# Performance work log

Hardware: AMD Instinct MI355X
Metric: run time of the kernel (lower is better)

## Reference

```python
import math
import jax, jax.numpy as jnp
import numpy as np

B, N, H, NH, DD, L = 4, 384, 256, 8, 32, 4
HD = H // NH
V = 11           # num_species + 1 (padding row 0)
CUTOFF = 5.0

def _ln(x, g, b):
    m = jnp.mean(x, axis=-1, keepdims=True)
    v = jnp.mean(jnp.square(x - m), axis=-1, keepdims=True)
    return (x - m) / jnp.sqrt(v + 1e-5) * g + b

def setup_inputs() -> dict:
    key = jax.random.key(0)
    ks = iter(jax.random.split(key, 64))
    def nrm(shape, s=0.05):
        return jax.random.normal(next(ks), shape, jnp.float32) * s
    return {
        'node_indices': jax.random.randint(next(ks), (B, N), 0, V),
        'positions': jax.random.normal(next(ks), (B, N, 3), jnp.float32),
        'mask': jnp.ones((B, N), jnp.float32),
        'emb': nrm((V, H)).at[0].set(0.0),
        'ln1_g': jnp.ones((L, H)), 'ln1_b': jnp.zeros((L, H)),
        'qkv_w': nrm((L, H, 3 * H)), 'qkv_b': jnp.zeros((L, 3 * H)),
        'out_w': nrm((L, H, H)), 'out_b': jnp.zeros((L, H)),
        'rb_w1': nrm((L, DD, H)), 'rb_b1': jnp.zeros((L, H)),
        'rb_w2': nrm((L, H, NH)), 'rb_b2': jnp.zeros((L, NH)),
        'gate_w1': nrm((L, H, H)), 'gate_b1': jnp.zeros((L, H)),
        'gate_w2': nrm((L, H, H)), 'gate_b2': jnp.zeros((L, H)),
        'ln2_g': jnp.ones((L, H)), 'ln2_b': jnp.zeros((L, H)),
        'ff_w1': nrm((L, H, 2 * H)), 'ff_b1': jnp.zeros((L, 2 * H)),
        'ff_w2': nrm((L, 2 * H, H)), 'ff_b2': jnp.zeros((L, H)),
        'pool_g': jnp.ones((H,)), 'pool_beta': jnp.zeros((H,)),
        'pool_w': nrm((H, H)), 'pool_b': jnp.zeros((H,)),
        'eh_w': nrm((H, 1)), 'eh_b': jnp.zeros((1,)),
    }

def _forward(node_indices, positions, mask, emb, ln1_g, ln1_b, qkv_w, qkv_b,
             out_w, out_b, rb_w1, rb_b1, rb_w2, rb_b2, gate_w1, gate_b1,
             gate_w2, gate_b2, ln2_g, ln2_b, ff_w1, ff_b1, ff_w2, ff_b2,
             pool_g, pool_beta, pool_w, pool_b, eh_w, eh_b):
    mask_b = mask > 0
    x = emb[node_indices] * mask_b[..., None]               # [B,N,H]
    pos = positions * mask_b[..., None].astype(positions.dtype)
    rel = pos[:, :, None, :] - pos[:, None, :, :]           # [B,N,N,3]
    dist = jnp.linalg.norm(rel + 1e-9, axis=-1)             # [B,N,N]
    adj = (dist <= CUTOFF).astype(jnp.float32)
    adj = adj * mask_b[:, None, :] * mask_b[:, :, None]
    edge = adj > 0
    isolated = mask_b & ~edge.any(axis=-1)
    adj = adj + isolated.astype(jnp.float32)[:, :, None] * jnp.eye(N, dtype=jnp.float32)
    edge = adj > 0
    # Bessel envelope features [B,N,N,DD]
    kk = jnp.arange(1, DD + 1, dtype=jnp.float32)
    ang = math.pi * kk * (dist / CUTOFF)[..., None]
    feat = jnp.sin(ang) / (dist[..., None] + 1e-6)
    feat = feat * (dist <= CUTOFF)[..., None].astype(jnp.float32)
    feat = feat * adj[..., None]

    scale = math.sqrt(HD)
    NEG = jnp.finfo(jnp.float32).min
    for l in range(L):
        res = x
        h = _ln(x, ln1_g[l], ln1_b[l])
        qkv = h @ qkv_w[l] + qkv_b[l]
        q, k, v = jnp.split(qkv, 3, axis=-1)
        q = q.reshape(B, N, NH, HD)
        k = k.reshape(B, N, NH, HD)
        v = v.reshape(B, N, NH, HD)
        logits = jnp.einsum('bihd,bjhd->bhij', q, k) / scale
        hb = jax.nn.silu(feat @ rb_w1[l] + rb_b1[l])        # [B,N,N,H]
        bias = hb @ rb_w2[l] + rb_b2[l]                     # [B,N,N,NH]
        logits = logits + bias.transpose(0, 3, 1, 2)
        logits = jnp.where(edge[:, None, :, :], logits, NEG)
        attn = jax.nn.softmax(logits, axis=-1)
        ctx = jnp.einsum('bhij,bjhd->bihd', attn, v).reshape(B, N, H)
        gated = jax.nn.silu(h @ gate_w1[l] + gate_b1[l]) @ gate_w2[l] + gate_b2[l]
        x = res + ((ctx * jax.nn.sigmoid(gated)) @ out_w[l] + out_b[l])
        y = _ln(x, ln2_g[l], ln2_b[l])
        x = x + (jax.nn.gelu(y @ ff_w1[l] + ff_b1[l], approximate=False) @ ff_w2[l] + ff_b2[l])

    pooled = jax.nn.silu(_ln(x, pool_g, pool_beta) @ pool_w + pool_b)
    masked = pooled * mask_b[..., None]
    counts = jnp.maximum(jnp.sum(mask_b, axis=1), 1)
    graph = jnp.sum(masked, axis=1) / counts[:, None]
    energy = (graph @ eh_w + eh_b)[:, 0]                    # [B]
    return energy

def reference(node_indices, positions, mask, emb, ln1_g, ln1_b, qkv_w, qkv_b,
              out_w, out_b, rb_w1, rb_b1, rb_w2, rb_b2, gate_w1, gate_b1,
              gate_w2, gate_b2, ln2_g, ln2_b, ff_w1, ff_b1, ff_w2, ff_b2,
              pool_g, pool_beta, pool_w, pool_b, eh_w, eh_b):
    return _forward(node_indices, positions, mask, emb, ln1_g, ln1_b, qkv_w,
                    qkv_b, out_w, out_b, rb_w1, rb_b1, rb_w2, rb_b2, gate_w1,
                    gate_b1, gate_w2, gate_b2, ln2_g, ln2_b, ff_w1, ff_b1,
                    ff_w2, ff_b2, pool_g, pool_beta, pool_w, pool_b, eh_w, eh_b)
```

## Files before the change

kernel.cpp:

```cpp
#include <hip/hip_runtime.h>
#include <hip/hip_bf16.h>
#include <math.h>

constexpr int B_ = 4, N_ = 384, H_ = 256, NH_ = 8, DD_ = 32, L_ = 4;
constexpr int M_ = B_ * N_;
constexpr float CUT = 5.0f;
constexpr float PI_ = 3.14159265358979323846f;
constexpr float INVSC = 0.17677669529663687f;
constexpr int TBL_N = 4096;
constexpr int TBL_STRIDE = 4098;

typedef __attribute__((ext_vector_type(8))) short short8;
typedef __attribute__((ext_vector_type(4))) float f32x4;
typedef __attribute__((ext_vector_type(4))) unsigned short u16x4;
using u16 = unsigned short;

__device__ __forceinline__ u16 f2b(float f) {
  __hip_bfloat16 h = __float2bfloat16(f);
  return *reinterpret_cast<u16*>(&h);
}
__device__ __forceinline__ float b2f(u16 u) {
  __hip_bfloat16 h;
  *reinterpret_cast<u16*>(&h) = u;
  return __bfloat162float(h);
}

__device__ __forceinline__ float wave_sum(float v) {
#pragma unroll
  for (int s = 1; s < 64; s <<= 1) v += __shfl_xor(v, s);
  return v;
}


__device__ __forceinline__ void bias_item(const float* __restrict__ pos,
                                          const float* __restrict__ mask,
                                          const float* __restrict__ tbl2,
                                          u16* __restrict__ biasb, int e) {
  int j = e % N_;
  int t = e / N_;
  int i = t % N_;
  int b = t / N_;
  float mi = mask[b * N_ + i], mj = mask[b * N_ + j];
  const float* pi = pos + (size_t)(b * N_ + i) * 3;
  const float* pj = pos + (size_t)(b * N_ + j) * 3;
  float dx = pi[0] - pj[0] + 1e-9f;
  float dy = pi[1] - pj[1] + 1e-9f;
  float dz = pi[2] - pj[2] + 1e-9f;
  float d = sqrtf(dx * dx + dy * dy + dz * dz);
  bool edge = (mi > 0.f && mj > 0.f) && (d <= CUT);
  size_t plane = (size_t)N_ * N_;
  size_t obase = (size_t)b * NH_ * plane + (size_t)i * N_ + j;
  size_t lstride = (size_t)B_ * NH_ * plane;
  if (edge) {
    int ixrow;
    float fr;
    if (i == j) {
      ixrow = TBL_N + 1;
      fr = 0.f;
    } else {
      float u = d * ((float)TBL_N / CUT);
      int ix = (int)u;
      ix = ix > TBL_N - 1 ? TBL_N - 1 : ix;
      fr = u - (float)ix;
      ixrow = ix;
    }
    const float4* r0 = (const float4*)(tbl2 + (size_t)ixrow * 32);
    const float4* r1 = (const float4*)(tbl2 + (size_t)(ixrow + 1) * 32);
    float4 a0[8], a1[8];
#pragma unroll
    for (int q = 0; q < 8; q++) {
      a0[q] = r0[q];
      a1[q] = r1[q];
    }
    float w0 = 1.f - fr;
#pragma unroll
    for (int q = 0; q < 8; q++) {
      float v0[4] = {a0[q].x, a0[q].y, a0[q].z, a0[q].w};
      float v1[4] = {a1[q].x, a1[q].y, a1[q].z, a1[q].w};
#pragma unroll
      for (int c = 0; c < 4; c++) {
        int lh = q * 4 + c;
        int l = lh >> 3, h = lh & 7;
        float v = v0[c] * w0 + v1[c] * fr;
        biasb[(size_t)l * lstride + obase + (size_t)h * plane] = f2b(v);
      }
    }
  } else {
#pragma unroll
    for (int lh = 0; lh < 32; lh++) {
      int l = lh >> 3, h = lh & 7;
      biasb[(size_t)l * lstride + obase + (size_t)h * plane] = 0xFF80;
    }
  }
}

struct TrJob {
  const float* src;
  u16* dst;
  int K, N, nx, ny, nz, base, dstride;
};
struct TrJobs {
  TrJob j[7];
};
__global__ __launch_bounds__(256) void setup_all_k(TrJobs jobs,
                                                   const float* __restrict__ rb_w1,
                                                   const float* __restrict__ rb_b1,
                                                   const float* __restrict__ rb_w2,
                                                   const float* __restrict__ rb_b2,
                                                   float* __restrict__ tbl2,
                                                   const int* __restrict__ nidx,
                                                   const float* __restrict__ mask,
                                                   const float* __restrict__ emb,
                                                   float* __restrict__ X,
                                                   const float* __restrict__ l1g,
                                                   const float* __restrict__ l1b,
                                                   u16* __restrict__ HB) {
  __shared__ float sfA[64][32];
  __shared__ float hbA[64][260];
  __shared__ float t[32][33];
  __shared__ float sw[8];
  int bid = blockIdx.x;
  int tid = threadIdx.x;
  if (bid < 260) {
    constexpr int TT = 64;
    int l = bid / 65;
    int t0 = (bid % 65) * TT;
#pragma unroll
    for (int m = 0; m < 8; m++) {
      int idx = m * 256 + tid;
      int tl = idx >> 5, k = idx & 31;
      int tt = t0 + tl;
      float d = (tt <= TBL_N) ? (tt * (CUT / (float)TBL_N)) : 1.7320508075688772e-9f;
      float ang = PI_ * (k + 1) * d * (1.f / CUT);
      sfA[tl][k] = sinf(ang) / (d + 1e-6f);
    }
    __syncthreads();
    float w1c[32];
    const float* w1 = rb_w1 + (size_t)l * DD_ * H_;
#pragma unroll
    for (int k = 0; k < 32; k++) w1c[k] = w1[k * H_ + tid];
    float b1v = rb_b1[l * H_ + tid];
    for (int tl = 0; tl < TT; tl++) {
      float pre = b1v;
      const float4* sfp = (const float4*)sfA[tl];
#pragma unroll
      for (int kq = 0; kq < 8; kq++) {
        float4 s4 = sfp[kq];
        pre += s4.x * w1c[kq * 4] + s4.y * w1c[kq * 4 + 1] + s4.z * w1c[kq * 4 + 2] +
               s4.w * w1c[kq * 4 + 3];
      }
      hbA[tl][tid] = pre / (1.f + __expf(-pre));
    }
    __syncthreads();
    const float* w2 = rb_w2 + (size_t)l * H_ * NH_;
    int o = tid & 7;
    float b2v = rb_b2[l * NH_ + o];
#pragma unroll
    for (int half = 0; half < 2; half++) {
      int tl = (tid >> 3) + half * 32;
      float acc = b2v;
      const float4* hp = (const float4*)hbA[tl];
#pragma unroll 4
      for (int hq = 0; hq < 64; hq++) {
        float4 h4 = hp[hq];
        acc += h4.x * w2[(hq * 4 + 0) * NH_ + o] + h4.y * w2[(hq * 4 + 1) * NH_ + o] +
               h4.z * w2[(hq * 4 + 2) * NH_ + o] + h4.w * w2[(hq * 4 + 3) * NH_ + o];
      }
      int tt = t0 + tl;
      if (tt <= TBL_STRIDE) tbl2[(size_t)tt * 32 + l * NH_ + o] = acc;
    }
  } else if (bid < 2884) {
    int tb = bid - 260;
    int ji = 0;
#pragma unroll
    for (int q = 1; q < 7; q++)
      if (tb >= jobs.j[q].base) ji = q;
    const TrJob& J = jobs.j[ji];
    int local = tb - J.base;
    int z = local / (J.nx * J.ny);
    int r2 = local % (J.nx * J.ny);
    int ky = r2 / J.nx, kx = r2 % J.nx;
    int n0 = kx * 32, k0 = ky * 32;
    const float* s = J.src + (size_t)z * J.K * J.N;
    u16* d = J.dst + (size_t)z * J.dstride;
    int r = tid >> 3, c4 = (tid & 7) * 4;
    float4 v = *(const float4*)(s + (size_t)(k0 + r) * J.N + n0 + c4);
    t[r][c4 + 0] = v.x;
    t[r][c4 + 1] = v.y;
    t[r][c4 + 2] = v.z;
    t[r][c4 + 3] = v.w;
    __syncthreads();
    u16x4 o;
    o[0] = f2b(t[c4 + 0][r]);
    o[1] = f2b(t[c4 + 1][r]);
    o[2] = f2b(t[c4 + 2][r]);
    o[3] = f2b(t[c4 + 3][r]);
    *(u16x4*)(d + (size_t)(n0 + r) * J.K + k0 + c4) = o;
  } else {
    int row = bid - 2884;
    float mb = mask[row] > 0.f ? 1.f : 0.f;
    float v = emb[nidx[row] * H_ + tid] * mb;
    X[(size_t)row * H_ + tid] = v;
    float s = wave_sum(v);
    float q = wave_sum(v * v);
    int wv = tid >> 6, ln = tid & 63;
    if (ln == 0) {
      sw[wv] = s;
      sw[4 + wv] = q;
    }
    __syncthreads();
    float ts = sw[0] + sw[1] + sw[2] + sw[3];
    float tq = sw[4] + sw[5] + sw[6] + sw[7];
    float m = ts * (1.f / 256.f);
    float rs = rsqrtf(tq * (1.f / 256.f) - m * m + 1e-5f);
    HB[(size_t)row * H_ + tid] = f2b((v - m) * rs * l1g[tid] + l1b[tid]);
  }
}

__global__ __launch_bounds__(256) void ln_k(const float* __restrict__ X,
                                            const float* __restrict__ g,
                                            const float* __restrict__ bta,
                                            u16* __restrict__ O) {
  int wave = threadIdx.x >> 6, lane = threadIdx.x & 63;
  int row = blockIdx.x * 4 + wave;
  const float* xr = X + (size_t)row * H_;
  float4 v = *(const float4*)(xr + lane * 4);
  float s = v.x + v.y + v.z + v.w;
  s = wave_sum(s);
  float m = s * (1.f / H_);
  float dx = v.x - m, dy = v.y - m, dz = v.z - m, dw = v.w - m;
  float vs = dx * dx + dy * dy + dz * dz + dw * dw;
  vs = wave_sum(vs);
  float rs = rsqrtf(vs * (1.f / H_) + 1e-5f);
  float4 gg = *(const float4*)(g + lane * 4);
  float4 bb = *(const float4*)(bta + lane * 4);
  u16x4 o;
  o[0] = f2b(dx * rs * gg.x + bb.x);
  o[1] = f2b(dy * rs * gg.y + bb.y);
  o[2] = f2b(dz * rs * gg.z + bb.z);
  o[3] = f2b(dw * rs * gg.w + bb.w);
  *(u16x4*)(O + (size_t)row * H_ + lane * 4) = o;
}

template <int ACT, bool RES, bool PRE, bool OBF>
__device__ __forceinline__ void mgemm_body(u16* __restrict__ As, u16* __restrict__ Bs,
                                           const void* __restrict__ Av,
                                           const u16* __restrict__ WT,
                                           const float* __restrict__ bias,
                                           const float* __restrict__ resid,
                                           void* __restrict__ Cv, int K, int Nc,
                                           int lda, const float* __restrict__ G,
                                           const float* __restrict__ bias2,
                                           int m0, int n0) {
  const int tid = threadIdx.x;
  const int wave = tid >> 6, lane = tid & 63;
  const int wr = wave >> 1, wc = wave & 1, lr = lane & 15, lg = lane >> 4;
  f32x4 acc[2][2] = {};
  const int srow = tid >> 2, sp = tid & 3;
  for (int k0 = 0; k0 < K; k0 += 128) {
#pragma unroll
    for (int s4 = 0; s4 < 4; s4++) {
      int s = sp * 4 + s4;
      int phys = s ^ (srow & 15);
      if (PRE) {
        const float* ap = (const float*)Av + (size_t)(m0 + srow) * lda + k0 + s * 8;
        const float* gp = G + (size_t)(m0 + srow) * lda + k0 + s * 8;
        float4 a0 = *(const float4*)ap;
        float4 a1 = *(const float4*)(ap + 4);
        float4 g0 = *(const float4*)gp;
        float4 g1 = *(const float4*)(gp + 4);
        short8 vv;
        vv[0] = (short)f2b(a0.x / (1.f + __expf(-g0.x)));
        vv[1] = (short)f2b(a0.y / (1.f + __expf(-g0.y)));
        vv[2] = (short)f2b(a0.z / (1.f + __expf(-g0.z)));
        vv[3] = (short)f2b(a0.w / (1.f + __expf(-g0.w)));
        vv[4] = (short)f2b(a1.x / (1.f + __expf(-g1.x)));
        vv[5] = (short)f2b(a1.y / (1.f + __expf(-g1.y)));
        vv[6] = (short)f2b(a1.z / (1.f + __expf(-g1.z)));
        vv[7] = (short)f2b(a1.w / (1.f + __expf(-g1.w)));
        *(short8*)&As[srow * 128 + phys * 8] = vv;
      } else {
        const u16* Ab = (const u16*)Av;
        short8 v = *(const short8*)(Ab + (size_t)(m0 + srow) * lda + k0 + s * 8);
        *(short8*)&As[srow * 128 + phys * 8] = v;
      }
      short8 w = *(const short8*)(WT + (size_t)(n0 + srow) * K + k0 + s * 8);
      *(short8*)&Bs[srow * 128 + phys * 8] = w;
    }
    __syncthreads();
#pragma unroll
    for (int kk = 0; kk < 4; kk++) {
      int slot = kk * 4 + lg;
      short8 af[2], bf_[2];
#pragma unroll
      for (int i = 0; i < 2; i++) {
        int row = wr * 32 + i * 16 + lr;
        af[i] = *(const short8*)&As[row * 128 + (slot ^ (row & 15)) * 8];
      }
#pragma unroll
      for (int j = 0; j < 2; j++) {
        int row = wc * 32 + j * 16 + lr;
        bf_[j] = *(const short8*)&Bs[row * 128 + (slot ^ (row & 15)) * 8];
      }
#pragma unroll
      for (int i = 0; i < 2; i++)
#pragma unroll
        for (int j = 0; j < 2; j++)
          acc[i][j] = __builtin_amdgcn_mfma_f32_16x16x32_bf16(af[i], bf_[j], acc[i][j], 0, 0, 0);
    }
    __syncthreads();
  }
#pragma unroll
  for (int i = 0; i < 2; i++)
#pragma unroll
    for (int j = 0; j < 2; j++)
#pragma unroll
      for (int rg = 0; rg < 4; rg++) {
        int row = m0 + wr * 32 + i * 16 + lg * 4 + rg;
        int col = n0 + wc * 32 + j * 16 + lr;
        float v;
        if (ACT == 3) {
          float bv = (col < 768) ? bias[col] : bias2[col - 768];
          v = acc[i][j][rg] + bv;
          if (col >= 768) v = v / (1.f + __expf(-v));
        } else {
          v = acc[i][j][rg] + bias[col];
          if (ACT == 1) v = v / (1.f + __expf(-v));
          if (ACT == 2) v = 0.5f * v * (1.f + erff(v * 0.70710678118654752f));
        }
        if (RES) v += resid[(size_t)row * Nc + col];
        if (OBF)
          ((u16*)Cv)[(size_t)row * Nc + col] = f2b(v);
        else
          ((float*)Cv)[(size_t)row * Nc + col] = v;
      }
}

template <int ACT, bool RES, bool PRE, bool OBF>
__global__ __launch_bounds__(256) void mgemm_k(const void* __restrict__ Av,
                                               const u16* __restrict__ WT,
                                               const float* __restrict__ bias,
                                               const float* __restrict__ resid,
                                               void* __restrict__ Cv, int K, int Nc,
                                               int lda, const float* __restrict__ G,
                                               const float* __restrict__ bias2) {
  __shared__ u16 As[64 * 128];
  __shared__ u16 Bs[64 * 128];
  mgemm_body<ACT, RES, PRE, OBF>(As, Bs, Av, WT, bias, resid, Cv, K, Nc, lda, G, bias2,
                                 blockIdx.y * 64, blockIdx.x * 64);
}

__global__ __launch_bounds__(256) void qkv_bias_k(const u16* __restrict__ hb,
                                                  const u16* __restrict__ wqg,
                                                  const float* __restrict__ qb,
                                                  const float* __restrict__ gb1,
                                                  u16* __restrict__ qgb,
                                                  const float* __restrict__ pos,
                                                  const float* __restrict__ mask,
                                                  const float* __restrict__ tbl2,
                                                  u16* __restrict__ biasb) {
  __shared__ u16 As[64 * 128];
  __shared__ u16 Bs[64 * 128];
  int bid = blockIdx.x;
  if (bid < 384) {
    mgemm_body<3, false, false, true>(As, Bs, hb, wqg, qb, nullptr, qgb, 256, 1024, 256,
                                      nullptr, gb1, (bid >> 4) * 64, (bid & 15) * 64);
  } else {
    bias_item(pos, mask, tbl2, biasb, (bid - 384) * 256 + threadIdx.x);
  }
}

__device__ __forceinline__ void attn_body(u16* __restrict__ FragQ, u16* __restrict__ FragK,
                                          u16* __restrict__ FragV, float* __restrict__ smax,
                                          float* __restrict__ ssum,
                                          const u16* __restrict__ qkv,
                                          const u16* __restrict__ biasb,
                                          float* __restrict__ ctx, int qs,
                                          int it, int hh, int b) {
  u16* FragP = FragK;
  float* pbuf = (float*)FragV;
  const int i0 = it * 32;
  const int tid = threadIdx.x;
  const size_t bb = (size_t)b * N_;

  if (tid < 128) {
    int q = tid >> 2, dc = tid & 3;
    short8 v = *(const short8*)(qkv + (bb + i0 + q) * qs + hh * 32 + dc * 8);
    *(short8*)&FragQ[(((q >> 4) * 64) + (q & 15) + 16 * dc) * 8] = v;
  }
#pragma unroll
  for (int m = 0; m < 6; m++) {
    int idx = m * 256 + tid;
    int key = idx >> 2, dc = idx & 3;
    const u16* kb = qkv + (bb + key) * qs + 256 + hh * 32 + dc * 8;
    short8 kv = *(const short8*)kb;
    *(short8*)&FragK[(((key >> 4) * 64) + (key & 15) + 16 * dc) * 8] = kv;
    short8 vv = *(const short8*)(kb + 256);
    int kc = key >> 5, sub = (key >> 3) & 3, kj = key & 7;
#pragma unroll
    for (int j = 0; j < 8; j++) {
      int d = dc * 8 + j;
      FragV[(((kc * 2 + (d >> 4)) * 64) + (d & 15) + 16 * sub) * 8 + kj] = (u16)vv[j];
    }
  }
  __syncthreads();

  const int wave = tid >> 6, lane = tid & 63;
  const int rh = wave & 1, kh = wave >> 1;
  const int g = lane >> 4, c = lane & 15;
  const u16* bptr = biasb + (size_t)(b * NH_ + hh) * N_ * N_;

  short8 qf = *(const short8*)&FragQ[(rh * 64 + lane) * 8];
  f32x4 sc[12];
#pragma unroll
  for (int t = 0; t < 12; t++) {
    int T = kh * 12 + t;
    short8 kf = *(const short8*)&FragK[(T * 64 + lane) * 8];
    f32x4 z = {0.f, 0.f, 0.f, 0.f};
    sc[t] = __builtin_amdgcn_mfma_f32_16x16x32_bf16(qf, kf, z, 0, 0, 0);
    int key = 16 * T + c;
#pragma unroll
    for (int reg = 0; reg < 4; reg++) {
      int row = i0 + 16 * rh + 4 * g + reg;
      float bv = b2f(bptr[(size_t)row * N_ + key]);
      sc[t][reg] = sc[t][reg] * INVSC + bv;
    }
  }
  float mx[4];
#pragma unroll
  for (int reg = 0; reg < 4; reg++) {
    float m = sc[0][reg];
#pragma unroll
    for (int t = 1; t < 12; t++) m = fmaxf(m, sc[t][reg]);
#pragma unroll
    for (int s = 1; s < 16; s <<= 1) m = fmaxf(m, __shfl_xor(m, s));
    mx[reg] = m;
  }
  if (c == 0) {
#pragma unroll
    for (int reg = 0; reg < 4; reg++) smax[kh * 32 + 16 * rh + 4 * g + reg] = mx[reg];
  }
  __syncthreads();
  float sm[4];
#pragma unroll
  for (int reg = 0; reg < 4; reg++) {
    float M = fmaxf(smax[16 * rh + 4 * g + reg], smax[32 + 16 * rh + 4 * g + reg]);
    float s = 0.f;
#pragma unroll
    for (int t = 0; t < 12; t++) {
      float p = __expf(sc[t][reg] - M);
      sc[t][reg] = p;
      s += p;
    }
    sm[reg] = s;
  }
#pragma unroll
  for (int reg = 0; reg < 4; reg++) {
#pragma unroll
    for (int s = 1; s < 16; s <<= 1) sm[reg] += __shfl_xor(sm[reg], s);
  }
  if (c == 0) {
#pragma unroll
    for (int reg = 0; reg < 4; reg++) ssum[kh * 32 + 16 * rh + 4 * g + reg] = sm[reg];
  }
#pragma unroll
  for (int t = 0; t < 12; t++) {
    int T = kh * 12 + t;
    int kc = T >> 1;
    int sub = (2 * T + (c >> 3)) & 3;
#pragma unroll
    for (int reg = 0; reg < 4; reg++) {
      FragP[((rh * 12 + kc) * 64 + (4 * g + reg) + 16 * sub) * 8 + (c & 7)] =
          f2b(sc[t][reg]);
    }
  }
  __syncthreads();
  float Ls[4];
#pragma unroll
  for (int reg = 0; reg < 4; reg++)
    Ls[reg] = ssum[16 * rh + 4 * g + reg] + ssum[32 + 16 * rh + 4 * g + reg];

  f32x4 pcc[2] = {};
#pragma unroll
  for (int t = 0; t < 6; t++) {
    int kc = kh * 6 + t;
    short8 pf = *(const short8*)&FragP[((rh * 12 + kc) * 64 + lane) * 8];
#pragma unroll
    for (int nh = 0; nh < 2; nh++) {
      short8 vf = *(const short8*)&FragV[((kc * 2 + nh) * 64 + lane) * 8];
      pcc[nh] = __builtin_amdgcn_mfma_f32_16x16x32_bf16(pf, vf, pcc[nh], 0, 0, 0);
    }
  }
  __syncthreads();
  if (kh == 1) {
#pragma unroll
    for (int nh = 0; nh < 2; nh++)
#pragma unroll
      for (int reg = 0; reg < 4; reg++)
        pbuf[rh * 512 + (4 * g + reg) * 32 + nh * 16 + c] = pcc[nh][reg];
  }
  __syncthreads();
  if (kh == 0) {
#pragma unroll
    for (int nh = 0; nh < 2; nh++)
#pragma unroll
      for (int reg = 0; reg < 4; reg++) {
        float v = pcc[nh][reg] + pbuf[rh * 512 + (4 * g + reg) * 32 + nh * 16 + c];
        int row = i0 + 16 * rh + 4 * g + reg;
        ctx[(bb + row) * H_ + hh * 32 + nh * 16 + c] = v / Ls[reg];
      }
  }
}

__global__ __launch_bounds__(256) void attn_g2_k(const u16* __restrict__ qkv,
                                                 const u16* __restrict__ biasb,
                                                 float* __restrict__ ctx,
                                                 const u16* __restrict__ wg2,
                                                 const float* __restrict__ gb2,
                                                 float* __restrict__ g2) {
  __shared__ __align__(16) u16 SMEM[(2 + 24 + 24) * 64 * 8];
  __shared__ float sred[2 * 32 * 2];
  int bid = blockIdx.x;
  if (bid < 384) {
    int it = bid % 12;
    int t = bid / 12;
    attn_body(SMEM, SMEM + 1024, SMEM + 1024 + 12288, sred, sred + 64,
              qkv, biasb, ctx, 1024, it, t % NH_, t / NH_);
  } else {
    int g = bid - 384;
    mgemm_body<0, false, false, false>(SMEM, SMEM + 8192, (const void*)(qkv + 768), wg2,
                                       gb2, nullptr, g2, 256, 256, 1024, nullptr,
                                       nullptr, (g >> 2) * 64, (g & 3) * 64);
  }
}

__global__ __launch_bounds__(256) void energy_k(const float* __restrict__ p2,
                                                const float* __restrict__ mask,
                                                const float* __restrict__ ehw,
                                                const float* __restrict__ ehb,
                                                float* __restrict__ out) {
  int b = blockIdx.x, h = threadIdx.x;
  float s = 0.f, cnt = 0.f;
#pragma unroll 4
  for (int i = 0; i < N_; i++) {
    float m = mask[b * N_ + i] > 0.f ? 1.f : 0.f;
    s += p2[(size_t)(b * N_ + i) * H_ + h] * m;
    cnt += m;
  }
  float val = s * ehw[h];
  __shared__ float red[256];
  red[h] = val;
  __syncthreads();
  for (int st = 128; st > 0; st >>= 1) {
    if (h < st) red[h] += red[h + st];
    __syncthreads();
  }
  if (h == 0) {
    float c = cnt < 1.f ? 1.f : cnt;
    out[b] = red[0] / c + ehb[0];
  }
}

extern "C" void kernel_launch(void* const* d_in, const int* in_sizes, int n_in,
                              void* d_out, int out_size, void* d_ws, size_t ws_size,
                              hipStream_t stream) {
  const int* node_idx = (const int*)d_in[0];
  const float* positions = (const float*)d_in[1];
  const float* mask = (const float*)d_in[2];
  const float* emb = (const float*)d_in[3];
  const float* ln1_g = (const float*)d_in[4];
  const float* ln1_b = (const float*)d_in[5];
  const float* qkv_w = (const float*)d_in[6];
  const float* qkv_b = (const float*)d_in[7];
  const float* out_w = (const float*)d_in[8];
  const float* out_b = (const float*)d_in[9];
  const float* rb_w1 = (const float*)d_in[10];
  const float* rb_b1 = (const float*)d_in[11];
  const float* rb_w2 = (const float*)d_in[12];
  const float* rb_b2 = (const float*)d_in[13];
  const float* gate_w1 = (const float*)d_in[14];
  const float* gate_b1 = (const float*)d_in[15];
  const float* gate_w2 = (const float*)d_in[16];
  const float* gate_b2 = (const float*)d_in[17];
  const float* ln2_g = (const float*)d_in[18];
  const float* ln2_b = (const float*)d_in[19];
  const float* ff_w1 = (const float*)d_in[20];
  const float* ff_b1 = (const float*)d_in[21];
  const float* ff_w2 = (const float*)d_in[22];
  const float* ff_b2 = (const float*)d_in[23];
  const float* pool_g = (const float*)d_in[24];
  const float* pool_beta = (const float*)d_in[25];
  const float* pool_w = (const float*)d_in[26];
  const float* pool_b = (const float*)d_in[27];
  const float* eh_w = (const float*)d_in[28];
  const float* eh_b = (const float*)d_in[29];
  float* eout = (float*)d_out;

  char* W8 = (char*)d_ws;
  float* x = (float*)(W8 + 0);
  u16* qgb = (u16*)(W8 + 1572864);
  float* ctx = (float*)(W8 + 4718592);
  float* g2 = (float*)(W8 + 6291456);
  u16* hb = (u16*)(W8 + 7864320);
  u16* ffb = (u16*)(W8 + 8650752);
  float* tbl2 = (float*)(W8 + 12582912);
  u16* wt = (u16*)(W8 + 13631488);
  u16* wt_qg = wt;
  u16* wt_out = wt + 1048576;
  u16* wt_g2 = wt + 1310720;
  u16* wt_f1 = wt + 1572864;
  u16* wt_f2 = wt + 2097152;
  u16* wt_p = wt + 2621440;
  u16* biasb = (u16*)(W8 + 19005440);
  const size_t bias_lstride = (size_t)B_ * NH_ * N_ * N_;

  {
    TrJobs jobs;
    jobs.j[0] = {qkv_w, wt_qg, 256, 768, 24, 8, 4, 0, 262144};
    jobs.j[1] = {gate_w1, wt_qg + 768 * 256, 256, 256, 8, 8, 4, 768, 262144};
    jobs.j[2] = {out_w, wt_out, 256, 256, 8, 8, 4, 1024, 65536};
    jobs.j[3] = {gate_w2, wt_g2, 256, 256, 8, 8, 4, 1280, 65536};
    jobs.j[4] = {ff_w1, wt_f1, 256, 512, 16, 8, 4, 1536, 131072};
    jobs.j[5] = {ff_w2, wt_f2, 512, 256, 8, 16, 4, 2048, 131072};
    jobs.j[6] = {pool_w, wt_p, 256, 256, 8, 8, 1, 2560, 65536};
    setup_all_k<<<4420, 256, 0, stream>>>(jobs, rb_w1, rb_b1, rb_w2, rb_b2, tbl2,
                                          node_idx, mask, emb, x, ln1_g, ln1_b, hb);
  }

  for (int l = 0; l < L_; l++) {
    const float* qb = qkv_b + (size_t)l * 3 * H_;
    const float* ob = out_b + (size_t)l * H_;
    const float* gb1 = gate_b1 + (size_t)l * H_;
    const float* gb2 = gate_b2 + (size_t)l * H_;
    const float* fb1 = ff_b1 + (size_t)l * 2 * H_;
    const float* fb2 = ff_b2 + (size_t)l * H_;
    u16* wqg = wt_qg + (size_t)l * 1024 * 256;
    u16* wo = wt_out + (size_t)l * 256 * 256;
    u16* wg2 = wt_g2 + (size_t)l * 256 * 256;
    u16* wf1 = wt_f1 + (size_t)l * 512 * 256;
    u16* wf2 = wt_f2 + (size_t)l * 256 * 512;

    if (l == 0) {
      qkv_bias_k<<<2688, 256, 0, stream>>>(hb, wqg, qb, gb1, qgb, positions, mask, tbl2,
                                           biasb);
    } else {
      mgemm_k<3, false, false, true><<<dim3(16, 24), 256, 0, stream>>>(
          hb, wqg, qb, nullptr, qgb, 256, 1024, 256, nullptr, gb1);
    }
    attn_g2_k<<<480, 256, 0, stream>>>(qgb, biasb + (size_t)l * bias_lstride, ctx,
                                       wg2, gb2, g2);
    mgemm_k<0, true, true, false><<<dim3(4, 24), 256, 0, stream>>>(
        ctx, wo, ob, x, x, 256, 256, 256, g2, nullptr);
    ln_k<<<M_ / 4, 256, 0, stream>>>(x, ln2_g + l * H_, ln2_b + l * H_, hb);
    mgemm_k<2, false, false, true><<<dim3(8, 24), 256, 0, stream>>>(
        hb, wf1, fb1, nullptr, ffb, 256, 512, 256, nullptr, nullptr);
    mgemm_k<0, true, false, false><<<dim3(4, 24), 256, 0, stream>>>(
        ffb, wf2, fb2, x, x, 512, 256, 512, nullptr, nullptr);
    const float* nlg = (l < 3) ? (ln1_g + (l + 1) * H_) : pool_g;
    const float* nlb = (l < 3) ? (ln1_b + (l + 1) * H_) : pool_beta;
    ln_k<<<M_ / 4, 256, 0, stream>>>(x, nlg, nlb, hb);
  }

  mgemm_k<1, false, false, false><<<dim3(4, 24), 256, 0, stream>>>(
      hb, wt_p, pool_b, nullptr, ctx, 256, 256, 256, nullptr, nullptr);
  energy_k<<<B_, 256, 0, stream>>>(ctx, mask, eh_w, eh_b, eout);
}
```

Before: 273.0 us.

## Fuse LayerNorm into GEMM prologues using per-row partial stats from epilogues

Removes the standalone LayerNorm kernels. Residual-producing GEMMs now emit per-row partial sums and sums of squares for each 64-column block, and the consuming GEMMs rebuild mean and rstd from these and normalize fp32 x while loading A tiles. This drops two launches per layer plus the bf16 round trip through the hb buffer. In exchange, the consuming GEMMs read fp32 instead of bf16 and recompute the normalization once per column block. Variance is computed as E[x²]−m², which is less numerically stable.

After: 327.4 us. 1.2x slower.

```diff
diff --git a/kernel.cpp b/kernel.cpp
--- a/kernel.cpp
+++ b/kernel.cpp
@@ -112,13 +112,10 @@
                                                    const float* __restrict__ mask,
                                                    const float* __restrict__ emb,
                                                    float* __restrict__ X,
-                                                   const float* __restrict__ l1g,
-                                                   const float* __restrict__ l1b,
-                                                   u16* __restrict__ HB) {
+                                                   float* __restrict__ pstats) {
   __shared__ float sfA[64][32];
   __shared__ float hbA[64][260];
   __shared__ float t[32][33];
-  __shared__ float sw[8];
   int bid = blockIdx.x;
   int tid = threadIdx.x;
   if (bid < 260) {
@@ -205,44 +202,13 @@
     float q = wave_sum(v * v);
     int wv = tid >> 6, ln = tid & 63;
     if (ln == 0) {
-      sw[wv] = s;
-      sw[4 + wv] = q;
-    }
-    __syncthreads();
-    float ts = sw[0] + sw[1] + sw[2] + sw[3];
-    float tq = sw[4] + sw[5] + sw[6] + sw[7];
-    float m = ts * (1.f / 256.f);
-    float rs = rsqrtf(tq * (1.f / 256.f) - m * m + 1e-5f);
-    HB[(size_t)row * H_ + tid] = f2b((v - m) * rs * l1g[tid] + l1b[tid]);
-  }
-}
-
-__global__ __launch_bounds__(256) void ln_k(const float* __restrict__ X,
-                                            const float* __restrict__ g,
-                                            const float* __restrict__ bta,
-                                            u16* __restrict__ O) {
-  int wave = threadIdx.x >> 6, lane = threadIdx.x & 63;
-  int row = blockIdx.x * 4 + wave;
-  const float* xr = X + (size_t)row * H_;
-  float4 v = *(const float4*)(xr + lane * 4);
-  float s = v.x + v.y + v.z + v.w;
-  s = wave_sum(s);
-  float m = s * (1.f / H_);
-  float dx = v.x - m, dy = v.y - m, dz = v.z - m, dw = v.w - m;
-  float vs = dx * dx + dy * dy + dz * dz + dw * dw;
-  vs = wave_sum(vs);
-  float rs = rsqrtf(vs * (1.f / H_) + 1e-5f);
-  float4 gg = *(const float4*)(g + lane * 4);
-  float4 bb = *(const float4*)(bta + lane * 4);
-  u16x4 o;
-  o[0] = f2b(dx * rs * gg.x + bb.x);
-  o[1] = f2b(dy * rs * gg.y + bb.y);
-  o[2] = f2b(dz * rs * gg.z + bb.z);
-  o[3] = f2b(dw * rs * gg.w + bb.w);
-  *(u16x4*)(O + (size_t)row * H_ + lane * 4) = o;
-}
-
-template <int ACT, bool RES, bool PRE, bool OBF>
+      pstats[(size_t)row * 8 + wv * 2 + 0] = s;
+      pstats[(size_t)row * 8 + wv * 2 + 1] = q;
+    }
+  }
+}
+
+template <int ACT, bool RES, bool PRE, bool OBF, bool LNS, bool STATS>
 __device__ __forceinline__ void mgemm_body(u16* __restrict__ As, u16* __restrict__ Bs,
                                            const void* __restrict__ Av,
                                            const u16* __restrict__ WT,
@@ -251,12 +217,29 @@
                                            void* __restrict__ Cv, int K, int Nc,
                                            int lda, const float* __restrict__ G,
                                            const float* __restrict__ bias2,
+                                           const float* __restrict__ lng,
+                                           const float* __restrict__ lnb,
+                                           const float* __restrict__ psin,
+                                           float* __restrict__ psout,
                                            int m0, int n0) {
   const int tid = threadIdx.x;
   const int wave = tid >> 6, lane = tid & 63;
   const int wr = wave >> 1, wc = wave & 1, lr = lane & 15, lg = lane >> 4;
   f32x4 acc[2][2] = {};
   const int srow = tid >> 2, sp = tid & 3;
+  float lnm = 0.f, lnrs = 0.f;
+  if (LNS) {
+    const float2* ps = (const float2*)(psin + (size_t)(m0 + srow) * 8);
+    float S = 0.f, Q = 0.f;
+#pragma unroll
+    for (int cb = 0; cb < 4; cb++) {
+      float2 p = ps[cb];
+      S += p.x;
+      Q += p.y;
+    }
+    lnm = S * (1.f / 256.f);
+    lnrs = rsqrtf(Q * (1.f / 256.f) - lnm * lnm + 1e-5f);
+  }
   for (int k0 = 0; k0 < K; k0 += 128) {
 #pragma unroll
     for (int s4 = 0; s4 < 4; s4++) {
@@ -265,19 +248,17 @@
       if (PRE) {
         const float* ap = (const float*)Av + (size_t)(m0 + srow) * lda + k0 + s * 8;
         const float* gp = G + (size_t)(m0 + srow) * lda + k0 + s * 8;
-        float4 a0 = *(const float4*)ap;
-        float4 a1 = *(const float4*)(ap + 4);
-        float4 g0 = *(const float4*)gp;
-        float4 g1 = *(const float4*)(gp + 4);
         short8 vv;
-        vv[0] = (short)f2b(a0.x / (1.f + __expf(-g0.x)));
-        vv[1] = (short)f2b(a0.y / (1.f + __expf(-g0.y)));
-        vv[2] = (short)f2b(a0.z / (1.f + __expf(-g0.z)));
-        vv[3] = (short)f2b(a0.w / (1.f + __expf(-g0.w)));
-        vv[4] = (short)f2b(a1.x / (1.f + __expf(-g1.x)));
-        vv[5] = (short)f2b(a1.y / (1.f + __expf(-g1.y)));
-        vv[6] = (short)f2b(a1.z / (1.f + __expf(-g1.z)));
-        vv[7] = (short)f2b(a1.w / (1.f + __expf(-g1.w)));
+#pragma unroll
+        for (int q = 0; q < 8; q++) vv[q] = (short)f2b(ap[q] / (1.f + __expf(-gp[q])));
+        *(short8*)&As[srow * 128 + phys * 8] = vv;
+      } else if (LNS) {
+        const float* ap = (const float*)Av + (size_t)(m0 + srow) * lda + k0 + s * 8;
+        int c0 = k0 + s * 8;
+        short8 vv;
+#pragma unroll
+        for (int q = 0; q < 8; q++)
+          vv[q] = (short)f2b((ap[q] - lnm) * lnrs * lng[c0 + q] + lnb[c0 + q]);
         *(short8*)&As[srow * 128 + phys * 8] = vv;
       } else {
         const u16* Ab = (const u16*)Av;
@@ -310,6 +291,7 @@
     }
     __syncthreads();
   }
+  float fv[2][2][4];
 #pragma unroll
   for (int i = 0; i < 2; i++)
 #pragma unroll
@@ -329,32 +311,69 @@
           if (ACT == 2) v = 0.5f * v * (1.f + erff(v * 0.70710678118654752f));
         }
         if (RES) v += resid[(size_t)row * Nc + col];
+        fv[i][j][rg] = v;
         if (OBF)
           ((u16*)Cv)[(size_t)row * Nc + col] = f2b(v);
         else
           ((float*)Cv)[(size_t)row * Nc + col] = v;
       }
-}
-
-template <int ACT, bool RES, bool PRE, bool OBF>
+  if (STATS) {
+    float* sst = (float*)As;
+#pragma unroll
+    for (int i = 0; i < 2; i++)
+#pragma unroll
+      for (int rg = 0; rg < 4; rg++) {
+        float s = fv[i][0][rg] + fv[i][1][rg];
+        float q = fv[i][0][rg] * fv[i][0][rg] + fv[i][1][rg] * fv[i][1][rg];
+#pragma unroll
+        for (int sh = 1; sh < 16; sh <<= 1) {
+          s += __shfl_xor(s, sh);
+          q += __shfl_xor(q, sh);
+        }
+        if (lr == 0) {
+          int row = wr * 32 + i * 16 + lg * 4 + rg;
+          sst[wc * 128 + row * 2 + 0] = s;
+          sst[wc * 128 + row * 2 + 1] = q;
+        }
+      }
+    __syncthreads();
+    if (tid < 64) {
+      float s = sst[tid * 2] + sst[128 + tid * 2];
+      float q = sst[tid * 2 + 1] + sst[128 + tid * 2 + 1];
+      int bx = n0 >> 6;
+      psout[(size_t)(m0 + tid) * 8 + bx * 2 + 0] = s;
+      psout[(size_t)(m0 + tid) * 8 + bx * 2 + 1] = q;
+    }
+  }
+}
+
+template <int ACT, bool RES, bool PRE, bool OBF, bool LNS, bool STATS>
 __global__ __launch_bounds__(256) void mgemm_k(const void* __restrict__ Av,
                                                const u16* __restrict__ WT,
                                                const float* __restrict__ bias,
                                                const float* __restrict__ resid,
                                                void* __restrict__ Cv, int K, int Nc,
                                                int lda, const float* __restrict__ G,
-                                               const float* __restrict__ bias2) {
+                                               const float* __restrict__ bias2,
+                                               const float* __restrict__ lng,
+                                               const float* __restrict__ lnb,
+                                               const float* __restrict__ psin,
+                                               float* __restrict__ psout) {
   __shared__ u16 As[64 * 128];
   __shared__ u16 Bs[64 * 128];
-  mgemm_body<ACT, RES, PRE, OBF>(As, Bs, Av, WT, bias, resid, Cv, K, Nc, lda, G, bias2,
-                                 blockIdx.y * 64, blockIdx.x * 64);
-}
-
-__global__ __launch_bounds__(256) void qkv_bias_k(const u16* __restrict__ hb,
+  mgemm_body<ACT, RES, PRE, OBF, LNS, STATS>(As, Bs, Av, WT, bias, resid, Cv, K, Nc, lda,
+                                             G, bias2, lng, lnb, psin, psout,
+                                             blockIdx.y * 64, blockIdx.x * 64);
+}
+
+__global__ __launch_bounds__(256) void qkv_bias_k(const float* __restrict__ x,
                                                   const u16* __restrict__ wqg,
                                                   const float* __restrict__ qb,
                                                   const float* __restrict__ gb1,
                                                   u16* __restrict__ qgb,
+                                                  const float* __restrict__ lng,
+                                                  const float* __restrict__ lnb,
+                                                  const float* __restrict__ pstats,
                                                   const float* __restrict__ pos,
                                                   const float* __restrict__ mask,
                                                   const float* __restrict__ tbl2,
@@ -363,8 +382,9 @@
   __shared__ u16 Bs[64 * 128];
   int bid = blockIdx.x;
   if (bid < 384) {
-    mgemm_body<3, false, false, true>(As, Bs, hb, wqg, qb, nullptr, qgb, 256, 1024, 256,
-                                      nullptr, gb1, (bid >> 4) * 64, (bid & 15) * 64);
+    mgemm_body<3, false, false, true, true, false>(
+        As, Bs, x, wqg, qb, nullptr, qgb, 256, 1024, 256, nullptr, gb1, lng, lnb,
+        pstats, nullptr, (bid >> 4) * 64, (bid & 15) * 64);
   } else {
     bias_item(pos, mask, tbl2, biasb, (bid - 384) * 256 + threadIdx.x);
   }
@@ -528,9 +548,10 @@
               qkv, biasb, ctx, 1024, it, t % NH_, t / NH_);
   } else {
     int g = bid - 384;
-    mgemm_body<0, false, false, false>(SMEM, SMEM + 8192, (const void*)(qkv + 768), wg2,
-                                       gb2, nullptr, g2, 256, 256, 1024, nullptr,
-                                       nullptr, (g >> 2) * 64, (g & 3) * 64);
+    mgemm_body<0, false, false, false, false, false>(
+        SMEM, SMEM + 8192, (const void*)(qkv + 768), wg2, gb2, nullptr, g2, 256, 256,
+        1024, nullptr, nullptr, nullptr, nullptr, nullptr, nullptr,
+        (g >> 2) * 64, (g & 3) * 64);
   }
 }
 
@@ -601,7 +622,7 @@
   u16* qgb = (u16*)(W8 + 1572864);
   float* ctx = (float*)(W8 + 4718592);
   float* g2 = (float*)(W8 + 6291456);
-  u16* hb = (u16*)(W8 + 7864320);
+  float* pstats = (float*)(W8 + 7864320);
   u16* ffb = (u16*)(W8 + 8650752);
   float* tbl2 = (float*)(W8 + 12582912);
   u16* wt = (u16*)(W8 + 13631488);
@@ -624,7 +645,7 @@
     jobs.j[5] = {ff_w2, wt_f2, 512, 256, 8, 16, 4, 2048, 131072};
     jobs.j[6] = {pool_w, wt_p, 256, 256, 8, 8, 1, 2560, 65536};
     setup_all_k<<<4420, 256, 0, stream>>>(jobs, rb_w1, rb_b1, rb_w2, rb_b2, tbl2,
-                                          node_idx, mask, emb, x, ln1_g, ln1_b, hb);
+                                          node_idx, mask, emb, x, pstats);
   }
 
   for (int l = 0; l < L_; l++) {
@@ -641,27 +662,29 @@
     u16* wf2 = wt_f2 + (size_t)l * 256 * 512;
 
     if (l == 0) {
-      qkv_bias_k<<<2688, 256, 0, stream>>>(hb, wqg, qb, gb1, qgb, positions, mask, tbl2,
-                                           biasb);
+      qkv_bias_k<<<2688, 256, 0, stream>>>(x, wqg, qb, gb1, qgb,
+                                           ln1_g, ln1_b, pstats,
+                                           positions, mask, tbl2, biasb);
     } else {
-      mgemm_k<3, false, false, true><<<dim3(16, 24), 256, 0, stream>>>(
-          hb, wqg, qb, nullptr, qgb, 256, 1024, 256, nullptr, gb1);
+      mgemm_k<3, false, false, true, true, false><<<dim3(16, 24), 256, 0, stream>>>(
+          x, wqg, qb, nullptr, qgb, 256, 1024, 256, nullptr, gb1,
+          ln1_g + l * H_, ln1_b + l * H_, pstats, nullptr);
     }
     attn_g2_k<<<480, 256, 0, stream>>>(qgb, biasb + (size_t)l * bias_lstride, ctx,
                                        wg2, gb2, g2);
-    mgemm_k<0, true, true, false><<<dim3(4, 24), 256, 0, stream>>>(
-        ctx, wo, ob, x, x, 256, 256, 256, g2, nullptr);
-    ln_k<<<M_ / 4, 256, 0, stream>>>(x, ln2_g + l * H_, ln2_b + l * H_, hb);
-    mgemm_k<2, false, false, true><<<dim3(8, 24), 256, 0, stream>>>(
-        hb, wf1, fb1, nullptr, ffb, 256, 512, 256, nullptr, nullptr);
-    mgemm_k<0, true, false, false><<<dim3(4, 24), 256, 0, stream>>>(
-        ffb, wf2, fb2, x, x, 512, 256, 512, nullptr, nullptr);
-    const float* nlg = (l < 3) ? (ln1_g + (l + 1) * H_) : pool_g;
-    const float* nlb = (l < 3) ? (ln1_b + (l + 1) * H_) : pool_beta;
-    ln_k<<<M_ / 4, 256, 0, stream>>>(x, nlg, nlb, hb);
-  }
-
-  mgemm_k<1, false, false, false><<<dim3(4, 24), 256, 0, stream>>>(
-      hb, wt_p, pool_b, nullptr, ctx, 256, 256, 256, nullptr, nullptr);
+    mgemm_k<0, true, true, false, false, true><<<dim3(4, 24), 256, 0, stream>>>(
+        ctx, wo, ob, x, x, 256, 256, 256, g2, nullptr, nullptr, nullptr, nullptr,
+        pstats);
+    mgemm_k<2, false, false, true, true, false><<<dim3(8, 24), 256, 0, stream>>>(
+        x, wf1, fb1, nullptr, ffb, 256, 512, 256, nullptr, nullptr,
+        ln2_g + l * H_, ln2_b + l * H_, pstats, nullptr);
+    mgemm_k<0, true, false, false, false, true><<<dim3(4, 24), 256, 0, stream>>>(
+        ffb, wf2, fb2, x, x, 512, 256, 512, nullptr, nullptr, nullptr, nullptr,
+        nullptr, pstats);
+  }
+
+  mgemm_k<1, false, false, false, true, false><<<dim3(4, 24), 256, 0, stream>>>(
+      x, wt_p, pool_b, nullptr, ctx, 256, 256, 256, nullptr, nullptr,
+      pool_g, pool_beta, pstats, nullptr);
   energy_k<<<B_, 256, 0, stream>>>(ctx, mask, eh_w, eh_b, eout);
 }
```
